# Kernel optimization log

Hardware: AMD Instinct MI355X
Metric: run time of the kernel (lower is better)

The kernel has to match this reference:

```python
import jax, jax.numpy as jnp
import numpy as np

N, E, D, ED, K = 16384, 524288, 64, 64, 16


def _lrelu(x, s):
    return jnp.where(x >= 0, x, s * x)


def _bn(x, g, b):
    # BatchNorm1d in training mode: biased batch statistics, eps=1e-5
    m = jnp.mean(x, axis=0)
    v = jnp.var(x, axis=0)
    return g * (x - m) * jax.lax.rsqrt(v + 1e-5) + b


def _segmax(msg, dst, n):
    # PyG aggr='max'; empty segments -> 0
    out = jax.ops.segment_max(msg, dst, num_segments=n)
    return jnp.where(jnp.isneginf(out), 0.0, out)


def _knn(x, k):
    # cosine kNN with self loops (bt_cosine=True, bt_self_loop=True)
    n = x.shape[0]
    xn = x * jax.lax.rsqrt(jnp.sum(x * x, axis=1, keepdims=True) + 1e-12)
    sim = jnp.where(jnp.eye(n, dtype=bool), -jnp.inf, xn @ xn.T)  # [n,n]
    idx = jax.lax.top_k(sim, k)[1]  # [n,k] sources j per target i
    loops = jnp.arange(n)
    src = jnp.concatenate([idx.reshape(-1), loops])
    dst = jnp.concatenate([jnp.repeat(loops, k), loops])
    return src, dst


def _static(x, src, dst, ea, w1, w2, w3, wl, n):
    # message: cat(x_j - x_i, edge_attr); scatter-max; update MLP (LeakyReLU 0.1)
    msg = jnp.concatenate([x[src] - x[dst], ea], axis=1)
    h = _segmax(msg, dst, n)
    h = _lrelu(h @ w1, 0.1)
    h = _lrelu(h @ w2, 0.1)
    h = _lrelu(h @ w3, 0.1)
    return _lrelu(x @ wl, 0.1) + h


def _dynamic(x, k, m1, m2, wl, n):
    # kNN recomputed under no_grad each call
    src, dst = _knn(jax.lax.stop_gradient(x), k)
    xi = x[dst]
    m = jnp.concatenate([xi, x[src] - xi], axis=1)
    m = _lrelu(m @ m1, 0.2)
    m = _lrelu(m @ m2, 0.2)
    return _lrelu(x @ wl, 0.1) + _segmax(m, dst, n)


def setup_inputs() -> dict:
    key = jax.random.key(0)
    ks = jax.random.split(key, 32)
    def w(i, shape):
        return jax.random.normal(ks[i], shape, dtype=jnp.float32) * 0.05
    return {
        'node_embedding': w(0, (N, D)),
        'edge_embedding': w(1, (E, ED)),
        'edge_index': jax.random.randint(ks[2], (2, E), 0, N),
        'k': K,
        'sg1_w1': w(3, (128, 96)), 'sg1_w2': w(4, (96, 64)), 'sg1_w3': w(5, (64, 64)), 'sg1_lin': w(6, (64, 64)),
        'sg2_w1': w(7, (128, 128)), 'sg2_w2': w(8, (128, 128)), 'sg2_w3': w(9, (128, 128)), 'sg2_lin': w(10, (64, 128)),
        'sg3_w1': w(11, (192, 192)), 'sg3_w2': w(12, (192, 192)), 'sg3_w3': w(13, (192, 192)), 'sg3_lin': w(14, (128, 192)),
        'dg1_m1': w(15, (128, 128)), 'dg1_m2': w(16, (128, 128)), 'dg1_lin': w(17, (64, 128)),
        'dg2_m1': w(18, (256, 192)), 'dg2_m2': w(19, (192, 192)), 'dg2_lin': w(20, (128, 192)),
        'f1_w': w(21, (704, 1024)), 'f1_g': jnp.ones(1024, jnp.float32), 'f1_b': jnp.zeros(1024, jnp.float32),
        'f2_w1': w(22, (1728, 512)), 'f2_g1': jnp.ones(512, jnp.float32), 'f2_b1': jnp.zeros(512, jnp.float32),
        'f2_w2': w(23, (512, 256)), 'f2_g2': jnp.ones(256, jnp.float32), 'f2_b2': jnp.zeros(256, jnp.float32),
        'f2_w3': w(24, (256, 128)),
    }


def reference(node_embedding, edge_embedding, edge_index, k,
              sg1_w1, sg1_w2, sg1_w3, sg1_lin,
              sg2_w1, sg2_w2, sg2_w3, sg2_lin,
              sg3_w1, sg3_w2, sg3_w3, sg3_lin,
              dg1_m1, dg1_m2, dg1_lin,
              dg2_m1, dg2_m2, dg2_lin,
              f1_w, f1_g, f1_b,
              f2_w1, f2_g1, f2_b1, f2_w2, f2_g2, f2_b2, f2_w3):
    n = node_embedding.shape[0]
    src, dst = edge_index[0], edge_index[1]
    sg1 = _static(node_embedding, src, dst, edge_embedding, sg1_w1, sg1_w2, sg1_w3, sg1_lin, n)
    sg2 = _static(sg1, src, dst, edge_embedding, sg2_w1, sg2_w2, sg2_w3, sg2_lin, n)
    sg3 = _static(sg2, src, dst, edge_embedding, sg3_w1, sg3_w2, sg3_w3, sg3_lin, n)
    dg1 = _dynamic(sg1, k, dg1_m1, dg1_m2, dg1_lin, n)
    dg2 = _dynamic(dg1, k, dg2_m1, dg2_m2, dg2_lin, n)
    cat1 = jnp.concatenate([sg1, dg1, dg2, sg2, sg3], axis=1)  # [N, 704]
    f1 = _lrelu(_bn(cat1 @ f1_w, f1_g, f1_b), 0.2)
    cat2 = jnp.concatenate([f1, cat1], axis=1)  # [N, 1728]
    h = _lrelu(_bn(cat2 @ f2_w1, f2_g1, f2_b1), 0.2)
    h = _lrelu(_bn(h @ f2_w2, f2_g2, f2_b2), 0.2)
    return h @ f2_w3  # [N, 128]
```

## Files before the change

kernel.cpp:

```cpp
#include <hip/hip_runtime.h>
#include <math.h>

typedef unsigned short u16;
typedef unsigned int u32;
typedef unsigned long long u64;
typedef __attribute__((ext_vector_type(8))) short short8v;
typedef __attribute__((ext_vector_type(4))) float f32x4;

static const int NN  = 16384;
static const int NE  = 524288;
static const int SCC = 1024;
static const int KEDGE = 17;

__device__ __forceinline__ u16 f2b(float v){
  u32 u = __float_as_uint(v);
  u += 0x7FFFu + ((u >> 16) & 1u);
  return (u16)(u >> 16);
}
__device__ __forceinline__ float b2f(u16 h){ return __uint_as_float(((u32)h) << 16); }

__device__ __forceinline__ void gl_lds16(const u16* g, u16* l){
  __builtin_amdgcn_global_load_lds(
      (const __attribute__((address_space(1))) u32*)(g),
      (__attribute__((address_space(3))) u32*)(l), 16, 0, 0);
}

__global__ void k_fill_i32(int* p, int v, int n){
  int i = blockIdx.x*256 + threadIdx.x; if (i < n) p[i] = v;
}
__global__ void k_split3(const float* __restrict__ s, u16* __restrict__ h,
                         u16* __restrict__ m, u16* __restrict__ l, int n,
                         int C, int ldo, int co, int ldl){
  int i = blockIdx.x*256 + threadIdx.x; if (i >= n) return;
  int r = i / C, c = i % C;
  float v = s[i];
  u16 hh = f2b(v);
  float rr = v - b2f(hh);
  u16 mm_ = f2b(rr);
  size_t o = (size_t)r*ldo + co + c;
  h[o] = hh; m[o] = mm_;
  if (l) l[(size_t)r*ldl + c] = f2b(rr - b2f(mm_));
}
__global__ void k_wprep3(const float* __restrict__ W, int K, int N, int Npad,
                         u16* __restrict__ h, u16* __restrict__ m, u16* __restrict__ l){
  int idx = blockIdx.x*256 + threadIdx.x; if (idx >= K*Npad) return;
  int n = idx / K, k = idx % K;
  float v = (n < N) ? W[(size_t)k*N + n] : 0.f;
  u16 hh = f2b(v); h[idx] = hh;
  float r = v - b2f(hh);
  u16 mm_ = f2b(r); m[idx] = mm_;
  l[idx] = f2b(r - b2f(mm_));
}

__global__ void k_hist(const int* __restrict__ dst, int* __restrict__ cnt){
  int e = blockIdx.x*256 + threadIdx.x; if (e < NE) atomicAdd(&cnt[dst[e]], 1);
}
__global__ void k_scan(const int* __restrict__ cnt, int* __restrict__ off){
  __shared__ int part[1024];
  int t = threadIdx.x;
  int base = t*16;
  int loc[16]; int s = 0;
#pragma unroll
  for (int q=0;q<16;q++){ loc[q] = s; s += cnt[base+q]; }
  part[t] = s; __syncthreads();
  for (int d=1; d<1024; d<<=1){
    int v = (t>=d) ? part[t-d] : 0; __syncthreads();
    part[t] += v; __syncthreads();
  }
  int prev = (t==0) ? 0 : part[t-1];
#pragma unroll
  for (int q=0;q<16;q++) off[base+q] = prev + loc[q];
  if (t == 1023) off[NN] = part[1023];
}
__global__ void k_csr_fill(const int* __restrict__ src, const int* __restrict__ dst,
                           const int* __restrict__ off, int* __restrict__ cur,
                           int* __restrict__ csrc, int* __restrict__ ceid){
  int e = blockIdx.x*256 + threadIdx.x; if (e >= NE) return;
  int d = dst[e];
  int p = atomicAdd(&cur[d], 1);
  int idx = off[d] + p;
  csrc[idx] = src[e];
  ceid[idx] = e;
}

__global__ void k_static_segmax(const float* __restrict__ x, int Dx,
                                const float* __restrict__ ea,
                                const int* __restrict__ off,
                                const int* __restrict__ csrc,
                                const int* __restrict__ ceid,
                                u16* __restrict__ th, u16* __restrict__ tm,
                                u16* __restrict__ tl){
  int i = blockIdx.x, c = threadIdx.x;
  int DM = Dx + 64;
  int s = off[i], e = off[i+1];
  float mx = -INFINITY;
  float v;
  if (c < Dx){
    for (int t = s; t < e; t++) mx = fmaxf(mx, x[(size_t)csrc[t]*Dx + c]);
    v = (s == e) ? 0.f : (mx - x[(size_t)i*Dx + c]);
  } else {
    int cc = c - Dx;
    for (int t = s; t < e; t++) mx = fmaxf(mx, ea[(size_t)ceid[t]*64 + cc]);
    v = (s == e) ? 0.f : mx;
  }
  size_t o = (size_t)i*DM + c;
  u16 h = f2b(v); th[o] = h;
  float r = v - b2f(h);
  u16 mm_ = f2b(r); tm[o] = mm_;
  tl[o] = f2b(r - b2f(mm_));
}

template<int P, int GATHER>
__global__ __launch_bounds__(256) void k_mgemm(
    const u16* __restrict__ Ah, const u16* __restrict__ Am, const u16* __restrict__ Al,
    int lda, int ldal,
    const u16* __restrict__ Bh, const u16* __restrict__ Bm, const u16* __restrict__ Bl,
    int ldb,
    float* __restrict__ Cf, u16* __restrict__ Ch, u16* __restrict__ Cm, u16* __restrict__ Cl,
    int ldc, int ldsp, int cosp, int ldspl,
    int K, int Nc, float slope, int flags, int colbase,
    const float* __restrict__ Xf, const int* __restrict__ topig, int c0g, int Dxg)
{
  constexpr int NC = (P == 3) ? 3 : 2;
  __shared__ u16 lds[NC*2*4096];
  const int t = threadIdx.x;
  const int m0 = blockIdx.y * 128, n0 = blockIdx.x * 128;
  const int wave = t >> 6, lane = t & 63;
  const int wr = (wave >> 1) << 6, wc = (wave & 1) << 6;
  const int l15 = lane & 15, l4 = lane >> 4;
  f32x4 acc[4][4] = {};

  const u16* Ap[3] = {Ah, Am, Al};
  const int ldav[3] = {lda, lda, ldal};
  const u16* Bp[3] = {Bh, Bm, Bl};

  const int c0c = wave*128 + lane, c1c = c0c + 64;
  const int r0c = c0c & 127, s0c = c0c >> 7;
  const int r1c = c1c & 127, s1c = c1c >> 7;
  const int lb0 = (wave*128)*8;
  const int lb1 = (wave*128 + 64)*8;

  size_t gA0[3], gA1[3], gB0[3], gB1[3];
#pragma unroll
  for (int cc=0; cc<NC; cc++){
    if (!GATHER){
      gA0[cc] = (size_t)(m0 + r0c)*ldav[cc] + s0c*8;
      gA1[cc] = (size_t)(m0 + r1c)*ldav[cc] + s1c*8;
    }
    gB0[cc] = (size_t)(n0 + r0c)*ldb + s0c*8;
    gB1[cc] = (size_t)(n0 + r1c)*ldb + s1c*8;
  }

  const int sr = t & 127, sseg = t >> 7;
  int node_i = 0, node_j = 0;
  if (GATHER){
    int erow = m0 + sr;
    int i = c0g + erow / KEDGE;
    int slot = erow % KEDGE;
    node_i = i;
    node_j = (slot < 16) ? topig[i*16 + slot] : i;
  }

  for (int k0 = 0; k0 < K; k0 += 32){
    __attribute__((aligned(16))) u16 hb[16], mb[16], lcb[16];
    if (GATHER){
      int kpos = k0 + sseg*16;
      bool side = kpos < Dxg;
      int kk = side ? kpos : kpos - Dxg;
      const float* xi = Xf + (size_t)node_i*Dxg + kk;
      const float* xj = Xf + (size_t)node_j*Dxg + kk;
#pragma unroll
      for (int q4=0;q4<4;q4++){
        float4 a = *(const float4*)(xi + q4*4);
        if (!side){
          float4 b = *(const float4*)(xj + q4*4);
          a = make_float4(b.x-a.x, b.y-a.y, b.z-a.z, b.w-a.w);
        }
        float vv[4] = {a.x, a.y, a.z, a.w};
#pragma unroll
        for (int q=0;q<4;q++){
          float v = vv[q];
          u16 h = f2b(v); hb[q4*4+q] = h;
          float r = v - b2f(h);
          u16 mm_ = f2b(r); mb[q4*4+q] = mm_;
          if (NC == 3) lcb[q4*4+q] = f2b(r - b2f(mm_));
        }
      }
    }
    __syncthreads();
    if (GATHER){
      int base0 = (sseg*2)*1024 + sr*8;
      int base1 = (sseg*2+1)*1024 + sr*8;
      *(int4*)&lds[0*4096 + base0] = *(const int4*)&hb[0];
      *(int4*)&lds[0*4096 + base1] = *(const int4*)&hb[8];
      *(int4*)&lds[1*4096 + base0] = *(const int4*)&mb[0];
      *(int4*)&lds[1*4096 + base1] = *(const int4*)&mb[8];
      if (NC == 3){
        *(int4*)&lds[2*4096 + base0] = *(const int4*)&lcb[0];
        *(int4*)&lds[2*4096 + base1] = *(const int4*)&lcb[8];
      }
    } else {
#pragma unroll
      for (int cc=0; cc<NC; cc++){
        gl_lds16(Ap[cc] + gA0[cc] + k0, &lds[cc*4096 + lb0]);
        gl_lds16(Ap[cc] + gA1[cc] + k0, &lds[cc*4096 + lb1]);
      }
    }
#pragma unroll
    for (int cc=0; cc<NC; cc++){
      gl_lds16(Bp[cc] + gB0[cc] + k0, &lds[(NC+cc)*4096 + lb0]);
      gl_lds16(Bp[cc] + gB1[cc] + k0, &lds[(NC+cc)*4096 + lb1]);
    }
    __syncthreads();
    short8v fa[NC][4], fb[NC][4];
#pragma unroll
    for (int m=0;m<4;m++){
      int ra = l4*1024 + (wr + m*16 + l15)*8;
      int rb = l4*1024 + (wc + m*16 + l15)*8;
#pragma unroll
      for (int cc=0;cc<NC;cc++){
        fa[cc][m] = *(const short8v*)&lds[cc*4096 + ra];
        fb[cc][m] = *(const short8v*)&lds[(NC+cc)*4096 + rb];
      }
    }
#pragma unroll
    for (int m=0;m<4;m++)
#pragma unroll
      for (int n=0;n<4;n++){
        if (P == 3){
          acc[m][n] = __builtin_amdgcn_mfma_f32_16x16x32_bf16(fa[1][m], fb[1][n], acc[m][n], 0,0,0);
          acc[m][n] = __builtin_amdgcn_mfma_f32_16x16x32_bf16(fa[0][m], fb[2][n], acc[m][n], 0,0,0);
          acc[m][n] = __builtin_amdgcn_mfma_f32_16x16x32_bf16(fa[2][m], fb[0][n], acc[m][n], 0,0,0);
        }
        acc[m][n] = __builtin_amdgcn_mfma_f32_16x16x32_bf16(fa[0][m], fb[1][n], acc[m][n], 0,0,0);
        acc[m][n] = __builtin_amdgcn_mfma_f32_16x16x32_bf16(fa[1][m], fb[0][n], acc[m][n], 0,0,0);
        acc[m][n] = __builtin_amdgcn_mfma_f32_16x16x32_bf16(fa[0][m], fb[0][n], acc[m][n], 0,0,0);
      }
  }

  const float NEG = -__builtin_inff();
#pragma unroll
  for (int n=0;n<4;n++){
    int col0 = n0 + wc + n*16;
    if (col0 >= Nc) continue;
    int col = col0 + l15;
#pragma unroll
    for (int m=0;m<4;m++){
      int rowb = m0 + wr + m*16 + l4*4;
#pragma unroll
      for (int r=0;r<4;r++){
        int row = rowb + r;
        float v = acc[m][n][r];
        if ((flags & 2) && row == colbase + col) v = NEG;
        else v = (v >= 0.f) ? v : v*slope;
        if (col < Nc){
          if (flags & 1) v += Cf[(size_t)row*ldc + col];
          if (Cf) Cf[(size_t)row*ldc + col] = v;
          if (Ch){
            size_t o = (size_t)row*ldsp + cosp + col;
            u16 h = f2b(v); Ch[o] = h;
            float rr = v - b2f(h);
            u16 mm_ = f2b(rr); Cm[o] = mm_;
            if (Cl) Cl[(size_t)row*ldspl + col] = f2b(rr - b2f(mm_));
          }
        }
      }
    }
  }
}

__global__ void k_normalize(const float* __restrict__ x,
                            u16* __restrict__ oh, u16* __restrict__ om,
                            u16* __restrict__ ol, int Dx){
  int i = blockIdx.x, lane = threadIdx.x;
  size_t o0 = (size_t)i*Dx + lane;
  float a = x[o0];
  float b = 0.f;
  if (Dx == 128) b = x[o0 + 64];
  float ss = a*a + b*b;
  for (int d = 32; d; d >>= 1) ss += __shfl_xor(ss, d);
  float rs = rsqrtf(ss + 1e-12f);
  float va = a*rs;
  u16 h = f2b(va); oh[o0] = h;
  float r = va - b2f(h);
  u16 mm_ = f2b(r); om[o0] = mm_;
  ol[o0] = f2b(r - b2f(mm_));
  if (Dx == 128){
    float vb = b*rs;
    u16 h2 = f2b(vb); oh[o0+64] = h2;
    float r2 = vb - b2f(h2);
    u16 m2 = f2b(r2); om[o0+64] = m2;
    ol[o0+64] = f2b(r2 - b2f(m2));
  }
}

__global__ void k_topk_merge(const float* __restrict__ S, int colbase,
                             float* __restrict__ topv, int* __restrict__ topi,
                             int first){
  const float INF = __builtin_inff();
  int i = blockIdx.x*4 + (threadIdx.x >> 6);
  int lane = threadIdx.x & 63;
  const float* row = S + (size_t)i * SCC;
  float cv[16]; int cj[16];
#pragma unroll
  for (int q4=0;q4<4;q4++){
    float4 v4 = *(const float4*)(row + lane*16 + q4*4);
    float vv[4] = {v4.x, v4.y, v4.z, v4.w};
#pragma unroll
    for (int q=0;q<4;q++){
      int j = colbase + lane*16 + q4*4 + q;
      float v = vv[q];
      if (j == i) v = -INF;
      cv[q4*4+q] = v; cj[q4*4+q] = j;
    }
  }
  float pv = -INF; int pj = 0x7fffffff;

  if (!first){
    if (lane < 16){ pv = topv[i*16+lane]; pj = topi[i*16+lane]; }
    float tv = __shfl(pv, 15); int tj = __shfl(pj, 15);
#pragma unroll
    for (int q=0;q<16;q++){
      bool surv = (cv[q] > tv) || (cv[q] == tv && cj[q] < tj);
      u64 msk = __ballot(surv);
      while (msk){
        int src = __ffsll((long long)msk) - 1; msk &= msk - 1;
        float v = __shfl(cv[q], src);
        int   j = __shfl(cj[q], src);
        if ((v > tv) || (v == tv && j < tj)){
          bool eb = (pv > v) || (pv == v && pj < j);
          u32 mb = (u32)__ballot(eb) & 0xFFFFu;
          int p = __popc(mb);
          float sv = __shfl_up(pv, 1); int sj = __shfl_up(pj, 1);
          if (lane < 16 && lane >= p){
            if (lane == p){ pv = v; pj = j; }
            else          { pv = sv; pj = sj; }
          }
          tv = __shfl(pv, 15); tj = __shfl(pj, 15);
        }
      }
    }
    if (lane < 16){ topv[i*16+lane] = pv; topi[i*16+lane] = pj; }
    return;
  }

  float myv = -INF; int myj = 0;
#pragma unroll
  for (int r=0;r<16;r++){
    float lv = pv; int lj = pj;
#pragma unroll
    for (int q=0;q<16;q++){
      bool better = (cv[q] > lv) || (cv[q] == lv && cj[q] < lj);
      if (better){ lv = cv[q]; lj = cj[q]; }
    }
    float bv = lv; int bj = lj;
    for (int d=32; d; d>>=1){
      float ov = __shfl_xor(bv, d);
      int oj = __shfl_xor(bj, d);
      bool better = (ov > bv) || (ov == bv && oj < bj);
      if (better){ bv = ov; bj = oj; }
    }
    if (lj == bj){
#pragma unroll
      for (int q=0;q<16;q++) if (cj[q] == bj) cv[q] = -INF;
    }
    if (lane == r){ myv = bv; myj = bj; }
  }
  if (lane < 16){ topv[i*16+lane] = myv; topi[i*16+lane] = myj; }
}

__global__ void k_segmax_add(const float* __restrict__ mo, int H2, int c0,
                             float* __restrict__ outp){
  int ii = blockIdx.x;
  int c = threadIdx.x;
  float m = -INFINITY;
  for (int s=0;s<KEDGE;s++) m = fmaxf(m, mo[(size_t)(ii*KEDGE+s)*H2 + c]);
  outp[(size_t)(c0+ii)*H2 + c] += m;
}

__global__ void k_bn_part(const float* __restrict__ X, int C,
                          float* __restrict__ psum, float* __restrict__ psq){
  int c = blockIdx.x*64 + (threadIdx.x & 63);
  int rl = threadIdx.x >> 6;
  int r0 = blockIdx.y * 512;
  float s = 0.f, q = 0.f;
  for (int r = r0 + rl; r < r0 + 512; r += 4){
    float v = X[(size_t)r*C + c];
    s += v; q += v*v;
  }
  __shared__ float ls[256], lq[256];
  ls[threadIdx.x] = s; lq[threadIdx.x] = q;
  __syncthreads();
  if (rl == 0){
    int tt = threadIdx.x;
    psum[blockIdx.y*C + c] = ls[tt] + ls[tt+64] + ls[tt+128] + ls[tt+192];
    psq [blockIdx.y*C + c] = lq[tt] + lq[tt+64] + lq[tt+128] + lq[tt+192];
  }
}
__global__ void k_bn_stats(const float* __restrict__ psum, const float* __restrict__ psq,
                           int C, float* __restrict__ stat){
  int c = blockIdx.x*256 + threadIdx.x; if (c >= C) return;
  float s = 0.f, q = 0.f;
  for (int ch=0; ch<32; ch++){ s += psum[ch*C + c]; q += psq[ch*C + c]; }
  float m = s * (1.f/16384.f);
  float var = q * (1.f/16384.f) - m*m;
  stat[c] = m;
  stat[C + c] = rsqrtf(var + 1e-5f);
}
__global__ void k_bn_apply(const float* __restrict__ X, int Cshift, int C,
                           const float* __restrict__ stat,
                           const float* __restrict__ g, const float* __restrict__ b,
                           u16* __restrict__ Oh, u16* __restrict__ Om,
                           int ldo, int co, int total){
  for (int idx = blockIdx.x*256 + threadIdx.x; idx < total; idx += gridDim.x*256){
    int c = idx & (C-1);
    int r = idx >> Cshift;
    float v = (X[idx] - stat[c]) * stat[C + c] * g[c] + b[c];
    v = (v >= 0.f) ? v : 0.2f*v;
    size_t o = (size_t)r*ldo + co + c;
    u16 h = f2b(v); Oh[o] = h;
    Om[o] = f2b(v - b2f(h));
  }
}

extern "C" void kernel_launch(void* const* d_in, const int* in_sizes, int n_in,
                              void* d_out, int out_size, void* d_ws, size_t ws_size,
                              hipStream_t stream) {
  (void)in_sizes; (void)n_in; (void)out_size; (void)ws_size;
  const float* x0   = (const float*)d_in[0];
  const float* ea   = (const float*)d_in[1];
  const int*   ei   = (const int*)d_in[2];
  const float* f1_g = (const float*)d_in[23];
  const float* f1_b = (const float*)d_in[24];
  const float* f2_g1= (const float*)d_in[26];
  const float* f2_b1= (const float*)d_in[27];
  const float* f2_g2= (const float*)d_in[29];
  const float* f2_b2= (const float*)d_in[30];
  float* out = (float*)d_out;

  const float* wsrc[22] = {
    (const float*)d_in[4],(const float*)d_in[5],(const float*)d_in[6],(const float*)d_in[7],
    (const float*)d_in[8],(const float*)d_in[9],(const float*)d_in[10],(const float*)d_in[11],
    (const float*)d_in[12],(const float*)d_in[13],(const float*)d_in[14],(const float*)d_in[15],
    (const float*)d_in[16],(const float*)d_in[17],(const float*)d_in[18],
    (const float*)d_in[19],(const float*)d_in[20],(const float*)d_in[21],
    (const float*)d_in[22],(const float*)d_in[25],(const float*)d_in[28],(const float*)d_in[31]
  };
  const int wK[22] = {128,96,64,64, 128,128,128,64, 192,192,192,128,
                      128,128,64, 256,192,128, 704, 1728, 512, 256};
  const int wN[22] = {96,64,64,64, 128,128,128,128, 192,192,192,192,
                      128,128,128, 192,192,192, 1024, 512, 256, 128};
  int wNp[22];
  for (int i=0;i<22;i++) wNp[i] = (wN[i] + 127) & ~127;

  char* w = (char*)d_ws;
  size_t off = 0;
  auto alloc = [&](size_t bytes)->char*{
    char* p = w + off; off = (off + bytes + 255) & ~(size_t)255; return p;
  };
  float* sg1f = (float*)alloc((size_t)NN*64*4);
  float* sg2f = (float*)alloc((size_t)NN*128*4);
  float* dg1f = (float*)alloc((size_t)NN*128*4);
  u16* cat1h = (u16*)alloc((size_t)NN*704*2);
  u16* cat1m = (u16*)alloc((size_t)NN*704*2);
  u16* sg1l  = (u16*)alloc((size_t)NN*64*2);
  u16* dg1l  = (u16*)alloc((size_t)NN*128*2);
  float* bnp  = (float*)alloc((size_t)2*32*1024*4);
  float* bns  = (float*)alloc((size_t)2*1024*4);
  u16 *wh[22], *wm[22], *wl[22];
  for (int i=0;i<22;i++){
    size_t e = (size_t)wK[i]*wNp[i];
    wh[i] = (u16*)alloc(e*2); wm[i] = (u16*)alloc(e*2); wl[i] = (u16*)alloc(e*2);
  }
  char* arena = alloc((size_t)120*1024*1024);
  size_t ac = 0;
  auto aalloc = [&](size_t b)->char*{
    char* p = arena + ac; ac = (ac + b + 255) & ~(size_t)255; return p;
  };

  auto MG = [&](int P, const u16* Ah, const u16* Am, const u16* Al, int lda, int ldal,
                const u16* Bh, const u16* Bm, const u16* Bl, int ldb,
                float* Cf, u16* Ch, u16* Cm, u16* Cl, int ldc, int ldsp, int cosp, int ldspl,
                int M, int K, int Nc, float slope, int flags, int colbase){
    dim3 g((Nc+127)/128, M/128);
    if (P == 3)
      k_mgemm<3,0><<<g,256,0,stream>>>(Ah,Am,Al,lda,ldal,Bh,Bm,Bl,ldb,
        Cf,Ch,Cm,Cl,ldc,ldsp,cosp,ldspl,K,Nc,slope,flags,colbase,nullptr,nullptr,0,0);
    else
      k_mgemm<2,0><<<g,256,0,stream>>>(Ah,Am,Al,lda,ldal,Bh,Bm,Bl,ldb,
        Cf,Ch,Cm,Cl,ldc,ldsp,cosp,ldspl,K,Nc,slope,flags,colbase,nullptr,nullptr,0,0);
  };
  auto MGG = [&](int P, const float* Xf, const int* topig, int c0g, int Dxg,
                 const u16* Bh, const u16* Bm, const u16* Bl, int ldb,
                 u16* Ch, u16* Cm, u16* Cl, int ldsp, int ldspl,
                 int M, int Nc, float slope){
    dim3 g((Nc+127)/128, M/128);
    if (P == 3)
      k_mgemm<3,1><<<g,256,0,stream>>>(nullptr,nullptr,nullptr,0,0,Bh,Bm,Bl,ldb,
        nullptr,Ch,Cm,Cl,0,ldsp,0,ldspl,2*Dxg,Nc,slope,0,0,Xf,topig,c0g,Dxg);
    else
      k_mgemm<2,1><<<g,256,0,stream>>>(nullptr,nullptr,nullptr,0,0,Bh,Bm,Bl,ldb,
        nullptr,Ch,Cm,Cl,0,ldsp,0,ldspl,2*Dxg,Nc,slope,0,0,Xf,topig,c0g,Dxg);
  };

  for (int i=0;i<22;i++){
    int e = wK[i]*wNp[i];
    k_wprep3<<<(e+255)/256, 256, 0, stream>>>(wsrc[i], wK[i], wN[i], wNp[i], wh[i], wm[i], wl[i]);
  }

  ac = 0;
  u16* t1s[3]; for (int c=0;c<3;c++) t1s[c] = (u16*)aalloc((size_t)NN*192*2);
  u16* t2s[3]; for (int c=0;c<3;c++) t2s[c] = (u16*)aalloc((size_t)NN*192*2);
  float* sof32 = (float*)aalloc((size_t)NN*192*4);
  int* csr_cnt = (int*)aalloc((size_t)NN*4);
  int* csr_off = (int*)aalloc((size_t)(NN+1)*4);
  int* csr_src = (int*)aalloc((size_t)NE*4);
  int* csr_eid = (int*)aalloc((size_t)NE*4);
  u16* x0s[3]; for (int c=0;c<3;c++) x0s[c] = (u16*)aalloc((size_t)NN*64*2);

  k_split3<<<(NN*64+255)/256, 256, 0, stream>>>(x0, x0s[0], x0s[1], x0s[2], NN*64, 64, 64, 0, 64);

  const int* srcp = ei;
  const int* dstp = ei + NE;
  k_fill_i32<<<(NN+255)/256, 256, 0, stream>>>(csr_cnt, 0, NN);
  k_hist<<<NE/256, 256, 0, stream>>>(dstp, csr_cnt);
  k_scan<<<1, 1024, 0, stream>>>(csr_cnt, csr_off);
  k_fill_i32<<<(NN+255)/256, 256, 0, stream>>>(csr_cnt, 0, NN);
  k_csr_fill<<<NE/256, 256, 0, stream>>>(srcp, dstp, csr_off, csr_cnt, csr_src, csr_eid);

  auto static_layer = [&](int P, const float* xf,
                          const u16* xh, const u16* xm, const u16* xl, int lda, int ldal,
                          int Dx, int wi, float* of, int co, u16* lout, int H1, int H2){
    int DM = Dx + 64;
    k_static_segmax<<<NN, DM, 0, stream>>>(xf, Dx, ea, csr_off, csr_src, csr_eid,
                                           t1s[0], t1s[1], t1s[2]);
    MG(P, t1s[0],t1s[1],t1s[2], DM,DM, wh[wi],wm[wi],wl[wi], DM,
       nullptr, t2s[0],t2s[1],t2s[2], 0, H1,0,H1, NN, DM, H1, 0.1f, 0, 0);
    MG(P, t2s[0],t2s[1],t2s[2], H1,H1, wh[wi+1],wm[wi+1],wl[wi+1], H1,
       nullptr, t1s[0],t1s[1],t1s[2], 0, H2,0,H2, NN, H1, H2, 0.1f, 0, 0);
    MG(P, xh,xm,xl, lda,ldal, wh[wi+3],wm[wi+3],wl[wi+3], Dx,
       of, nullptr,nullptr,nullptr, H2,0,0,0, NN, Dx, H2, 0.1f, 0, 0);
    MG(P, t1s[0],t1s[1],t1s[2], H2,H2, wh[wi+2],wm[wi+2],wl[wi+2], H2,
       of, cat1h,cat1m,lout, H2, 704,co,(lout? (co==0?64:128) : 0),
       NN, H2, H2, 0.1f, 1, 0);
  };
  static_layer(3, x0,  x0s[0],x0s[1],x0s[2], 64,64, 64, 0, sg1f, 0,   sg1l, 96, 64);
  static_layer(2, sg1f, cat1h+0,  cat1m+0,  nullptr, 704,0, 64, 4, sg2f, 384, nullptr, 128, 128);
  static_layer(2, sg2f, cat1h+384,cat1m+384,nullptr, 704,0, 128,8, sof32,512, nullptr, 192, 192);

  ac = 0;
  u16* xns[3]; for (int c=0;c<3;c++) xns[c] = (u16*)aalloc((size_t)NN*128*2);
  float* topv = (float*)aalloc((size_t)NN*16*4);
  int*   topi = (int*)aalloc((size_t)NN*16*4);
  float* dg2of = (float*)aalloc((size_t)NN*192*4);
  size_t dyn0 = ac;

  auto dyn_layer = [&](int P, const float* xf,
                       const u16* xh, const u16* xm, const u16* xl, int lda, int ldal,
                       int Dx, int wi, float* ofp, int co, u16* lout, int H1, int H2, int nch){
    const int R = nch*KEDGE;
    ac = dyn0;
    float* S = (float*)aalloc((size_t)NN*SCC*4);
    ac = dyn0;
    u16* mms[3]; for (int c=0;c<3;c++) mms[c] = (u16*)aalloc((size_t)R*H1*2);
    float* mout = (float*)aalloc((size_t)R*H2*4);

    k_normalize<<<NN, 64, 0, stream>>>(xf, xns[0], xns[1], xns[2], Dx);
    for (int cb = 0; cb < NN; cb += SCC){
      MG(3, xns[0],xns[1],xns[2], Dx,Dx,
         xns[0]+(size_t)cb*Dx, xns[1]+(size_t)cb*Dx, xns[2]+(size_t)cb*Dx, Dx,
         S, nullptr,nullptr,nullptr, SCC,0,0,0, NN, Dx, SCC, 1.0f, 2, cb);
      k_topk_merge<<<NN/4, 256, 0, stream>>>(S, cb, topv, topi, cb == 0);
    }
    MG(P, xh,xm,xl, lda,ldal, wh[wi+2],wm[wi+2],wl[wi+2], Dx,
       ofp, nullptr,nullptr,nullptr, H2,0,0,0, NN, Dx, H2, 0.1f, 0, 0);
    for (int c0 = 0; c0 < NN; c0 += nch){
      MGG(P, xf, topi, c0, Dx, wh[wi],wm[wi],wl[wi], 2*Dx,
          mms[0],mms[1],(P==3?mms[2]:nullptr), H1,H1, R, H1, 0.2f);
      MG(P, mms[0],mms[1],mms[2], H1,H1, wh[wi+1],wm[wi+1],wl[wi+1], H1,
         mout, nullptr,nullptr,nullptr, H2,0,0,0, R, H1, H2, 0.2f, 0, 0);
      k_segmax_add<<<nch, H2, 0, stream>>>(mout, H2, c0, ofp);
    }
    k_split3<<<(NN*H2+255)/256, 256, 0, stream>>>(ofp, cat1h, cat1m, lout,
                                                  NN*H2, H2, 704, co, H2);
  };
  dyn_layer(3, sg1f, cat1h+0, cat1m+0, sg1l, 704,64, 64,  12, dg1f, 64,  dg1l, 128, 128, 4096);
  dyn_layer(2, dg1f, cat1h+64,cat1m+64,nullptr,704,0, 128, 15, dg2of,192, nullptr,192, 192, 2048);

  ac = 0;
  u16*   f1sh = (u16*)aalloc((size_t)NN*1024*2);
  u16*   f1sm = (u16*)aalloc((size_t)NN*1024*2);
  float* fscr = (float*)aalloc((size_t)NN*512*4);
  u16* h2h = f1sh;
  u16* h2m = f1sm;
  float* h3f32 = (float*)(f1sm + (size_t)NN*512);
  u16* h3h = f1sh + (size_t)NN*512;
  u16* h3m = h3h + (size_t)NN*256;

  auto bn = [&](const float* X, int C, int Cshift, const float* g, const float* b,
                u16* Oh, u16* Om, int ldo, int co){
    k_bn_part<<<dim3(C/64, 32), 256, 0, stream>>>(X, C, bnp, bnp + 32*1024);
    k_bn_stats<<<(C+255)/256, 256, 0, stream>>>(bnp, bnp + 32*1024, C, bns);
    k_bn_apply<<<2048, 256, 0, stream>>>(X, Cshift, C, bns, g, b, Oh, Om, ldo, co, NN*C);
  };

  for (int p = 0; p < 2; p++){
    MG(2, cat1h,cat1m,nullptr, 704,0, wh[18]+(size_t)p*512*704, wm[18]+(size_t)p*512*704, nullptr, 704,
       fscr, nullptr,nullptr,nullptr, 512,0,0,0, NN, 704, 512, 1.f, 0, 0);
    bn(fscr, 512, 9, f1_g + p*512, f1_b + p*512, f1sh, f1sm, 1024, p*512);
  }
  MG(2, f1sh,f1sm,nullptr, 1024,0, wh[19],wm[19],nullptr, 1728,
     fscr, nullptr,nullptr,nullptr, 512,0,0,0, NN, 1024, 512, 1.f, 0, 0);
  MG(2, cat1h,cat1m,nullptr, 704,0, wh[19]+1024,wm[19]+1024,nullptr, 1728,
     fscr, nullptr,nullptr,nullptr, 512,0,0,0, NN, 704, 512, 1.f, 1, 0);
  bn(fscr, 512, 9, f2_g1, f2_b1, h2h, h2m, 512, 0);
  MG(2, h2h,h2m,nullptr, 512,0, wh[20],wm[20],nullptr, 512,
     h3f32, nullptr,nullptr,nullptr, 256,0,0,0, NN, 512, 256, 1.f, 0, 0);
  bn(h3f32, 256, 8, f2_g2, f2_b2, h3h, h3m, 256, 0);
  MG(2, h3h,h3m,nullptr, 256,0, wh[21],wm[21],nullptr, 256,
     out, nullptr,nullptr,nullptr, 128,0,0,0, NN, 256, 128, 1.f, 0, 0);
}
```

Baseline: 4.386 ms.

## Prune kNN top-k merge using per-64-column block maxima from GEMM epilogue

The similarity GEMM epilogue now computes each row's maximum over every 64-column half-tile and writes it to a small Smax buffer. It also skips storing rows whose block max falls below the current 16th-best value. The top-k merge kernel reads only the 64-column blocks whose max can beat the current threshold, and the first chunk now uses an iterative wave argmax over one block. This cuts global stores and reads of the NN x 1024 similarity buffer and the merge work, at the cost of extra shuffles and a reduction in the GEMM epilogue.

```diff
diff --git a/kernel.cpp b/kernel.cpp
--- a/kernel.cpp
+++ b/kernel.cpp
@@ -119,7 +119,8 @@
     float* __restrict__ Cf, u16* __restrict__ Ch, u16* __restrict__ Cm, u16* __restrict__ Cl,
     int ldc, int ldsp, int cosp, int ldspl,
     int K, int Nc, float slope, int flags, int colbase,
-    const float* __restrict__ Xf, const int* __restrict__ topig, int c0g, int Dxg)
+    const float* __restrict__ Xf, const int* __restrict__ topig, int c0g, int Dxg,
+    float* __restrict__ Smax, const float* __restrict__ TopvRO)
 {
   constexpr int NC = (P == 3) ? 3 : 2;
   __shared__ u16 lds[NC*2*4096];
@@ -239,6 +240,39 @@
   }
 
   const float NEG = -__builtin_inff();
+
+  float rmx[4][4], tpv[4][4];
+  if (Smax != nullptr){
+#pragma unroll
+    for (int m=0;m<4;m++)
+#pragma unroll
+      for (int r=0;r<4;r++){
+        int row = m0 + wr + m*16 + l4*4 + r;
+        float x = NEG;
+#pragma unroll
+        for (int n=0;n<4;n++){
+          int col = n0 + wc + n*16 + l15;
+          float v = acc[m][n][r];
+          if (row == colbase + col) v = NEG;
+          x = fmaxf(x, v);
+        }
+        x = fmaxf(x, __shfl_xor(x, 1));
+        x = fmaxf(x, __shfl_xor(x, 2));
+        x = fmaxf(x, __shfl_xor(x, 4));
+        x = fmaxf(x, __shfl_xor(x, 8));
+        rmx[m][r] = x;
+        tpv[m][r] = (colbase > 0) ? TopvRO[(size_t)row*16 + 15] : NEG;
+      }
+    if (l15 == 0){
+      int half = (n0 + wc) >> 6;
+#pragma unroll
+      for (int m=0;m<4;m++)
+#pragma unroll
+        for (int r=0;r<4;r++)
+          Smax[(size_t)(m0 + wr + m*16 + l4*4 + r)*16 + half] = rmx[m][r];
+    }
+  }
+
 #pragma unroll
   for (int n=0;n<4;n++){
     int col0 = n0 + wc + n*16;
@@ -249,6 +283,7 @@
       int rowb = m0 + wr + m*16 + l4*4;
 #pragma unroll
       for (int r=0;r<4;r++){
+        if (Smax != nullptr && colbase > 0 && rmx[m][r] < tpv[m][r]) continue;
         int row = rowb + r;
         float v = acc[m][n][r];
         if ((flags & 2) && row == colbase + col) v = NEG;
@@ -294,79 +329,69 @@
   }
 }
 
-__global__ void k_topk_merge(const float* __restrict__ S, int colbase,
+__global__ void k_topk_merge(const float* __restrict__ S,
+                             const float* __restrict__ Smax, int colbase,
                              float* __restrict__ topv, int* __restrict__ topi,
                              int first){
   const float INF = __builtin_inff();
   int i = blockIdx.x*4 + (threadIdx.x >> 6);
   int lane = threadIdx.x & 63;
   const float* row = S + (size_t)i * SCC;
-  float cv[16]; int cj[16];
-#pragma unroll
-  for (int q4=0;q4<4;q4++){
-    float4 v4 = *(const float4*)(row + lane*16 + q4*4);
-    float vv[4] = {v4.x, v4.y, v4.z, v4.w};
-#pragma unroll
-    for (int q=0;q<4;q++){
-      int j = colbase + lane*16 + q4*4 + q;
-      float v = vv[q];
-      if (j == i) v = -INF;
-      cv[q4*4+q] = v; cj[q4*4+q] = j;
-    }
-  }
+
   float pv = -INF; int pj = 0x7fffffff;
-
-  if (!first){
+  int start_h = 0;
+  if (first){
+    float cv = row[lane];
+    int cj = colbase + lane;
+    if (cj == i) cv = -INF;
+    float myv = -INF; int myj = 0x7fffffff;
+#pragma unroll
+    for (int r=0;r<16;r++){
+      float bv = cv; int bj = cj;
+      for (int d=32; d; d>>=1){
+        float ov = __shfl_xor(bv, d); int oj = __shfl_xor(bj, d);
+        if ((ov > bv) || (ov == bv && oj < bj)){ bv = ov; bj = oj; }
+      }
+      if (cj == bj) cv = -INF;
+      if (lane == r){ myv = bv; myj = bj; }
+    }
+    if (lane < 16){ pv = myv; pj = myj; }
+    start_h = 1;
+  } else {
     if (lane < 16){ pv = topv[i*16+lane]; pj = topi[i*16+lane]; }
-    float tv = __shfl(pv, 15); int tj = __shfl(pj, 15);
-#pragma unroll
-    for (int q=0;q<16;q++){
-      bool surv = (cv[q] > tv) || (cv[q] == tv && cj[q] < tj);
-      u64 msk = __ballot(surv);
-      while (msk){
-        int src = __ffsll((long long)msk) - 1; msk &= msk - 1;
-        float v = __shfl(cv[q], src);
-        int   j = __shfl(cj[q], src);
-        if ((v > tv) || (v == tv && j < tj)){
-          bool eb = (pv > v) || (pv == v && pj < j);
-          u32 mb = (u32)__ballot(eb) & 0xFFFFu;
-          int p = __popc(mb);
-          float sv = __shfl_up(pv, 1); int sj = __shfl_up(pj, 1);
-          if (lane < 16 && lane >= p){
-            if (lane == p){ pv = v; pj = j; }
-            else          { pv = sv; pj = sj; }
-          }
-          tv = __shfl(pv, 15); tj = __shfl(pj, 15);
+  }
+  float tv = __shfl(pv, 15); int tj = __shfl(pj, 15);
+
+  float sm = (lane < 16) ? Smax[(size_t)i*16 + lane] : -INF;
+  bool qual = (lane < 16) && (lane >= start_h) && (sm >= tv);
+  u64 qm = __ballot(qual);
+  bool dirty = (first != 0);
+  while (qm){
+    int h = __ffsll((long long)qm) - 1; qm &= qm - 1;
+    float v = row[h*64 + lane];
+    int j = colbase + h*64 + lane;
+    if (j == i) v = -INF;
+    bool sv = (v > tv) || (v == tv && j < tj);
+    u64 msk = __ballot(sv);
+    while (msk){
+      int src = __ffsll((long long)msk) - 1; msk &= msk - 1;
+      float vv = __shfl(v, src);
+      int   jj = __shfl(j, src);
+      if ((vv > tv) || (vv == tv && jj < tj)){
+        bool eb = (pv > vv) || (pv == vv && pj < jj);
+        u32 mb = (u32)__ballot(eb) & 0xFFFFu;
+        int p = __popc(mb);
+        float svv = __shfl_up(pv, 1); int sjj = __shfl_up(pj, 1);
+        if (lane < 16 && lane >= p){
+          if (lane == p){ pv = vv; pj = jj; }
+          else          { pv = svv; pj = sjj; }
         }
-      }
-    }
-    if (lane < 16){ topv[i*16+lane] = pv; topi[i*16+lane] = pj; }
-    return;
-  }
-
-  float myv = -INF; int myj = 0;
-#pragma unroll
-  for (int r=0;r<16;r++){
-    float lv = pv; int lj = pj;
-#pragma unroll
-    for (int q=0;q<16;q++){
-      bool better = (cv[q] > lv) || (cv[q] == lv && cj[q] < lj);
-      if (better){ lv = cv[q]; lj = cj[q]; }
-    }
-    float bv = lv; int bj = lj;
-    for (int d=32; d; d>>=1){
-      float ov = __shfl_xor(bv, d);
-      int oj = __shfl_xor(bj, d);
-      bool better = (ov > bv) || (ov == bv && oj < bj);
-      if (better){ bv = ov; bj = oj; }
-    }
-    if (lj == bj){
-#pragma unroll
-      for (int q=0;q<16;q++) if (cj[q] == bj) cv[q] = -INF;
-    }
-    if (lane == r){ myv = bv; myj = bj; }
-  }
-  if (lane < 16){ topv[i*16+lane] = myv; topi[i*16+lane] = myj; }
+        tv = __shfl(pv, 15); tj = __shfl(pj, 15);
+        dirty = true;
+      }
+    }
+  }
+  if (dirty && lane < 16){ topv[i*16+lane] = pv; topi[i*16+lane] = pj; }
 }
 
 __global__ void k_segmax_add(const float* __restrict__ mo, int H2, int c0,
@@ -485,10 +510,12 @@
     dim3 g((Nc+127)/128, M/128);
     if (P == 3)
       k_mgemm<3,0><<<g,256,0,stream>>>(Ah,Am,Al,lda,ldal,Bh,Bm,Bl,ldb,
-        Cf,Ch,Cm,Cl,ldc,ldsp,cosp,ldspl,K,Nc,slope,flags,colbase,nullptr,nullptr,0,0);
+        Cf,Ch,Cm,Cl,ldc,ldsp,cosp,ldspl,K,Nc,slope,flags,colbase,nullptr,nullptr,0,0,
+        nullptr,nullptr);
     else
       k_mgemm<2,0><<<g,256,0,stream>>>(Ah,Am,Al,lda,ldal,Bh,Bm,Bl,ldb,
-        Cf,Ch,Cm,Cl,ldc,ldsp,cosp,ldspl,K,Nc,slope,flags,colbase,nullptr,nullptr,0,0);
+        Cf,Ch,Cm,Cl,ldc,ldsp,cosp,ldspl,K,Nc,slope,flags,colbase,nullptr,nullptr,0,0,
+        nullptr,nullptr);
   };
   auto MGG = [&](int P, const float* Xf, const int* topig, int c0g, int Dxg,
                  const u16* Bh, const u16* Bm, const u16* Bl, int ldb,
@@ -497,10 +524,12 @@
     dim3 g((Nc+127)/128, M/128);
     if (P == 3)
       k_mgemm<3,1><<<g,256,0,stream>>>(nullptr,nullptr,nullptr,0,0,Bh,Bm,Bl,ldb,
-        nullptr,Ch,Cm,Cl,0,ldsp,0,ldspl,2*Dxg,Nc,slope,0,0,Xf,topig,c0g,Dxg);
+        nullptr,Ch,Cm,Cl,0,ldsp,0,ldspl,2*Dxg,Nc,slope,0,0,Xf,topig,c0g,Dxg,
+        nullptr,nullptr);
     else
       k_mgemm<2,1><<<g,256,0,stream>>>(nullptr,nullptr,nullptr,0,0,Bh,Bm,Bl,ldb,
-        nullptr,Ch,Cm,Cl,0,ldsp,0,ldspl,2*Dxg,Nc,slope,0,0,Xf,topig,c0g,Dxg);
+        nullptr,Ch,Cm,Cl,0,ldsp,0,ldspl,2*Dxg,Nc,slope,0,0,Xf,topig,c0g,Dxg,
+        nullptr,nullptr);
   };
 
   for (int i=0;i<22;i++){
@@ -552,6 +581,7 @@
   u16* xns[3]; for (int c=0;c<3;c++) xns[c] = (u16*)aalloc((size_t)NN*128*2);
   float* topv = (float*)aalloc((size_t)NN*16*4);
   int*   topi = (int*)aalloc((size_t)NN*16*4);
+  float* Smaxb = (float*)aalloc((size_t)NN*16*4);
   float* dg2of = (float*)aalloc((size_t)NN*192*4);
   size_t dyn0 = ac;
 
@@ -567,10 +597,12 @@
 
     k_normalize<<<NN, 64, 0, stream>>>(xf, xns[0], xns[1], xns[2], Dx);
     for (int cb = 0; cb < NN; cb += SCC){
-      MG(3, xns[0],xns[1],xns[2], Dx,Dx,
+      dim3 g(SCC/128, NN/128);
+      k_mgemm<3,0><<<g,256,0,stream>>>(xns[0],xns[1],xns[2], Dx,Dx,
          xns[0]+(size_t)cb*Dx, xns[1]+(size_t)cb*Dx, xns[2]+(size_t)cb*Dx, Dx,
-         S, nullptr,nullptr,nullptr, SCC,0,0,0, NN, Dx, SCC, 1.0f, 2, cb);
-      k_topk_merge<<<NN/4, 256, 0, stream>>>(S, cb, topv, topi, cb == 0);
+         S, nullptr,nullptr,nullptr, SCC,0,0,0, Dx, SCC, 1.0f, 2, cb,
+         nullptr,nullptr,0,0, Smaxb, topv);
+      k_topk_merge<<<NN/4, 256, 0, stream>>>(S, Smaxb, cb, topv, topi, cb == 0);
     }
     MG(P, xh,xm,xl, lda,ldal, wh[wi+2],wm[wi+2],wl[wi+2], Dx,
        ofp, nullptr,nullptr,nullptr, H2,0,0,0, NN, Dx, H2, 0.1f, 0, 0);
```

New measurement: 4.480 ms. 2.1% more time.
